# Kernel optimization log

Measured on AMD Instinct MI355X. Metric: run time of the kernel, lower is better.

## Reference

```python
import jax, jax.numpy as jnp
import numpy as np

D_MODEL = 768; HEADS = 12; DEPTH = 12; PATCH = 16; IMG = 224; NCLS = 1000
N_PATCH = (IMG // PATCH) ** 2  # 196
N_TOK = N_PATCH + 1            # 197 (cls token)
REGION = 16                    # tokens per routing region
TOPK = 4                       # regions gathered per query region


def layernorm(x, g, b, eps=1e-5):
    mu = jnp.mean(x, -1, keepdims=True)
    var = jnp.mean((x - mu) ** 2, -1, keepdims=True)
    return (x - mu) * jax.lax.rsqrt(var + eps) * g + b


def biformer_attn(h, qkv_w, qkv_b, proj_w, proj_b):
    # Bi-Level Routing Attention: region-mean routing + top-k region gather.
    B, N, C = h.shape
    dh = C // HEADS
    qkv = h @ qkv_w + qkv_b                      # [B,N,3C]
    pad = (-N) % REGION
    qkv = jnp.pad(qkv, ((0, 0), (0, pad), (0, 0)))
    Np = N + pad; R = Np // REGION
    q, k, v = jnp.split(qkv, 3, axis=-1)
    qr = q.reshape(B, R, REGION, C)
    kr = k.reshape(B, R, REGION, C)
    vr = v.reshape(B, R, REGION, C)
    # coarse region-level affinity from region means
    q_reg = qr.mean(2); k_reg = kr.mean(2)       # [B,R,C]
    aff = jnp.einsum('brc,bsc->brs', q_reg, k_reg)
    _, idx = jax.lax.top_k(aff, TOPK)            # [B,R,TOPK] int32
    gather = jax.vmap(lambda t, i: t[i])         # gather regions per batch elem
    kg = gather(kr, idx).reshape(B, R, TOPK * REGION, C)
    vg = gather(vr, idx).reshape(B, R, TOPK * REGION, C)
    # fine-grained attention within each region over gathered keys
    qh = qr.reshape(B, R, REGION, HEADS, dh)
    kh = kg.reshape(B, R, TOPK * REGION, HEADS, dh)
    vh = vg.reshape(B, R, TOPK * REGION, HEADS, dh)
    att = jnp.einsum('brmhd,brnhd->bhrmn', qh, kh) * (dh ** -0.5)
    att = jax.nn.softmax(att, axis=-1)
    out = jnp.einsum('bhrmn,brnhd->brmhd', att, vh).reshape(B, Np, C)[:, :N]
    return out @ proj_w + proj_b


def _forward(x, conv_w, conv_b, cls_token, pos_embed,
             ln1_g, ln1_b, qkv_w, qkv_b, proj_w, proj_b,
             ln2_g, ln2_b, fc1_w, fc1_b, fc2_w, fc2_b, head_w, head_b):
    B = x.shape[0]
    p = jax.lax.conv_general_dilated(
        x, conv_w, (PATCH, PATCH), 'VALID',
        dimension_numbers=('NCHW', 'OIHW', 'NCHW')) + conv_b[None, :, None, None]
    t = p.reshape(B, D_MODEL, N_PATCH).transpose(0, 2, 1)   # [B,196,C]
    t = jnp.concatenate([jnp.broadcast_to(cls_token, (B, 1, D_MODEL)), t], axis=1)
    t = t + pos_embed                                        # [B,197,C]

    def block(xc, pp):
        g1, b1, qw, qb, pw, pb, g2, b2, f1w, f1b, f2w, f2b = pp
        h = layernorm(xc, g1, b1)
        h = biformer_attn(h, qw, qb, pw, pb)
        h = layernorm(h, g2, b2)
        h = jax.nn.gelu(h @ f1w + f1b, approximate=False) @ f2w + f2b
        return xc + h, None   # single residual around LN-Attn-LN-MLP (as in source)

    blk = (ln1_g, ln1_b, qkv_w, qkv_b, proj_w, proj_b,
           ln2_g, ln2_b, fc1_w, fc1_b, fc2_w, fc2_b)
    t, _ = jax.lax.scan(block, t, blk)
    return t[:, 0] @ head_w + head_b


def setup_inputs() -> dict:
    key = jax.random.key(0)
    ks = jax.random.split(key, 10)
    B = 16; s = 0.02
    f32 = jnp.float32
    return {
        'x': jax.random.normal(ks[0], (B, 3, IMG, IMG), f32),
        'conv_w': jax.random.normal(ks[1], (D_MODEL, 3, PATCH, PATCH), f32) * s,
        'conv_b': jnp.zeros((D_MODEL,), f32),
        'cls_token': jax.random.normal(ks[2], (1, 1, D_MODEL), f32) * s,
        'pos_embed': jax.random.normal(ks[3], (1, N_TOK, D_MODEL), f32) * s,
        'ln1_g': jnp.ones((DEPTH, D_MODEL), f32),
        'ln1_b': jnp.zeros((DEPTH, D_MODEL), f32),
        'qkv_w': jax.random.normal(ks[4], (DEPTH, D_MODEL, 3 * D_MODEL), f32) * s,
        'qkv_b': jnp.zeros((DEPTH, 3 * D_MODEL), f32),
        'proj_w': jax.random.normal(ks[5], (DEPTH, D_MODEL, D_MODEL), f32) * s,
        'proj_b': jnp.zeros((DEPTH, D_MODEL), f32),
        'ln2_g': jnp.ones((DEPTH, D_MODEL), f32),
        'ln2_b': jnp.zeros((DEPTH, D_MODEL), f32),
        'fc1_w': jax.random.normal(ks[6], (DEPTH, D_MODEL, 4 * D_MODEL), f32) * s,
        'fc1_b': jnp.zeros((DEPTH, 4 * D_MODEL), f32),
        'fc2_w': jax.random.normal(ks[7], (DEPTH, 4 * D_MODEL, D_MODEL), f32) * s,
        'fc2_b': jnp.zeros((DEPTH, D_MODEL), f32),
        'head_w': jax.random.normal(ks[8], (D_MODEL, NCLS), f32) * s,
        'head_b': jnp.zeros((NCLS,), f32),
    }


def reference(x, conv_w, conv_b, cls_token, pos_embed,
              ln1_g, ln1_b, qkv_w, qkv_b, proj_w, proj_b,
              ln2_g, ln2_b, fc1_w, fc1_b, fc2_w, fc2_b, head_w, head_b):
    return _forward(x, conv_w, conv_b, cls_token, pos_embed,
                    ln1_g, ln1_b, qkv_w, qkv_b, proj_w, proj_b,
                    ln2_g, ln2_b, fc1_w, fc1_b, fc2_w, fc2_b, head_w, head_b)
```

## Files before the change

### kernel.cpp

```cpp
#include <hip/hip_runtime.h>
#include <hip/hip_bf16.h>
#include <math.h>


typedef __bf16 bf16_t;
typedef __bf16 bf16x8 __attribute__((ext_vector_type(8)));
typedef __bf16 bf16x4 __attribute__((ext_vector_type(4)));
typedef __bf16 bf16x2v __attribute__((ext_vector_type(2)));
typedef float floatx4 __attribute__((ext_vector_type(4)));

static __device__ __forceinline__ float b2f(bf16_t x) { return (float)x; }
static __device__ __forceinline__ bf16_t f2b(float x) { return (bf16_t)x; }

#define AS1q __attribute__((address_space(1)))
#define AS3q __attribute__((address_space(3)))
static __device__ __forceinline__ void gll16(const bf16_t* g, bf16_t* l) {
    __builtin_amdgcn_global_load_lds((const AS1q void*)g, (AS3q void*)l, 16, 0, 0);
}

__global__ void transpose_split(const float* __restrict__ in, bf16_t* __restrict__ oh,
                                bf16_t* __restrict__ ol, int R, int C) {
    __shared__ float tile[32][33];
    int c0 = blockIdx.x * 32, r0 = blockIdx.y * 32;
    int tx = threadIdx.x, ty = threadIdx.y;
#pragma unroll
    for (int i = 0; i < 4; i++) {
        int r = r0 + ty + i * 8;
        float v = 0.f;
        if (r < R && (c0 + tx) < C) v = in[(size_t)r * C + c0 + tx];
        tile[ty + i * 8][tx] = v;
    }
    __syncthreads();
#pragma unroll
    for (int i = 0; i < 4; i++) {
        int c = c0 + ty + i * 8;
        if (c < C && (r0 + tx) < R) {
            float v = tile[tx][ty + i * 8];
            bf16_t h = f2b(v);
            oh[(size_t)c * R + r0 + tx] = h;
            ol[(size_t)c * R + r0 + tx] = f2b(v - b2f(h));
        }
    }
}

__global__ void split_kernel(const float* __restrict__ in, bf16_t* __restrict__ oh,
                             bf16_t* __restrict__ ol, int n) {
    int id = blockIdx.x * 256 + threadIdx.x;
    if (id < n) {
        float v = in[id];
        bf16_t h = f2b(v);
        oh[id] = h;
        ol[id] = f2b(v - b2f(h));
    }
}

__global__ void im2col_split(const float* __restrict__ x, bf16_t* __restrict__ oh,
                             bf16_t* __restrict__ ol) {
    int id = blockIdx.x * 256 + threadIdx.x;
    if (id >= 3136 * 768) return;
    int col = id % 768, row = id / 768;
    int b = row / 196, p = row % 196;
    int py = p / 14, px = p % 14;
    int c = col >> 8, rem = col & 255, ky = rem >> 4, kx = rem & 15;
    float v = x[(((size_t)(b * 3 + c)) * 224 + (py * 16 + ky)) * 224 + (px * 16 + kx)];
    bf16_t h = f2b(v);
    oh[id] = h;
    ol[id] = f2b(v - b2f(h));
}

__global__ void clspos_kernel(const float* __restrict__ cls, const float* __restrict__ pos,
                              float* __restrict__ t) {
    int id = blockIdx.x * 256 + threadIdx.x;
    int b = id / 768, c = id % 768;
    t[((size_t)(b * 197)) * 768 + c] = cls[c] + pos[c];
}

__global__ __launch_bounds__(256) void ln_kernel(const float* __restrict__ in,
                                                 const float* __restrict__ g,
                                                 const float* __restrict__ bb,
                                                 bf16_t* __restrict__ oh,
                                                 bf16_t* __restrict__ ol,
                                                 float* __restrict__ outf) {
    int row = blockIdx.x;
    int t = threadIdx.x;
    const float* x = in + (size_t)row * 768;
    float v0 = x[t], v1 = x[t + 256], v2 = x[t + 512];
    float s = v0 + v1 + v2;
#pragma unroll
    for (int off = 32; off > 0; off >>= 1) s += __shfl_down(s, off, 64);
    __shared__ float red[8];
    int lane = t & 63, wave = t >> 6;
    if (lane == 0) red[wave] = s;
    __syncthreads();
    float mu = (red[0] + red[1] + red[2] + red[3]) * (1.f / 768.f);
    float d0 = v0 - mu, d1 = v1 - mu, d2 = v2 - mu;
    float vs = d0 * d0 + d1 * d1 + d2 * d2;
#pragma unroll
    for (int off = 32; off > 0; off >>= 1) vs += __shfl_down(vs, off, 64);
    if (lane == 0) red[4 + wave] = vs;
    __syncthreads();
    float var = (red[4] + red[5] + red[6] + red[7]) * (1.f / 768.f);
    float rstd = 1.0f / sqrtf(var + 1e-5f);
    float y0 = d0 * rstd * g[t] + bb[t];
    float y1 = d1 * rstd * g[t + 256] + bb[t + 256];
    float y2 = d2 * rstd * g[t + 512] + bb[t + 512];
    size_t base = (size_t)row * 768;
    bf16_t h0 = f2b(y0), h1 = f2b(y1), h2 = f2b(y2);
    oh[base + t] = h0; oh[base + t + 256] = h1; oh[base + t + 512] = h2;
    ol[base + t] = f2b(y0 - b2f(h0));
    ol[base + t + 256] = f2b(y1 - b2f(h1));
    ol[base + t + 512] = f2b(y2 - b2f(h2));
    if (outf) {
        outf[base + t] = y0; outf[base + t + 256] = y1; outf[base + t + 512] = y2;
    }
}

__global__ __launch_bounds__(256) void gemm_nts(const bf16_t* __restrict__ Ah,
                                                const bf16_t* __restrict__ Al,
                                                const bf16_t* __restrict__ Bh,
                                                const bf16_t* __restrict__ Bl,
                                                const float* __restrict__ bias,
                                                float* __restrict__ outF,
                                                bf16_t* __restrict__ outHi,
                                                bf16_t* __restrict__ outLo,
                                                int M, int N, int K, int Kc, int mode) {
    __shared__ __align__(16) bf16_t Ash[128 * 32];
    __shared__ __align__(16) bf16_t Asl[128 * 32];
    __shared__ __align__(16) bf16_t Bsh[128 * 32];
    __shared__ __align__(16) bf16_t Bsl[128 * 32];
    const int t = threadIdx.x;
    const int lane = t & 63, wave = t >> 6;
    const int quad = lane >> 4, l16 = lane & 15;
    const int wm = (wave >> 1) * 64, wn = (wave & 1) * 64;
    const int m0 = blockIdx.y * 128, n0 = blockIdx.x * 128;
    const int kz = blockIdx.z;

    floatx4 acc[4][4];
#pragma unroll
    for (int i = 0; i < 4; i++)
#pragma unroll
        for (int j = 0; j < 4; j++)
#pragma unroll
            for (int p = 0; p < 4; p++) acc[i][j][p] = 0.f;

    const int sr = wave * 16 + (lane >> 2);
    const int sc = (lane & 3) * 8;
    const size_t a0 = (size_t)(m0 + sr) * K + sc;
    const size_t a1 = (size_t)(m0 + 64 + sr) * K + sc;
    const size_t b0 = (size_t)(n0 + sr) * K + sc;
    const size_t b1 = (size_t)(n0 + 64 + sr) * K + sc;
    const int lo0 = wave * 512;
    const int lo1 = 2048 + wave * 512;

    const int kend = kz * Kc + Kc;
    for (int k0 = kz * Kc; k0 < kend; k0 += 32) {
        __syncthreads();
        gll16(Ah + a0 + k0, Ash + lo0);
        gll16(Ah + a1 + k0, Ash + lo1);
        gll16(Al + a0 + k0, Asl + lo0);
        gll16(Al + a1 + k0, Asl + lo1);
        gll16(Bh + b0 + k0, Bsh + lo0);
        gll16(Bh + b1 + k0, Bsh + lo1);
        gll16(Bl + b0 + k0, Bsl + lo0);
        gll16(Bl + b1 + k0, Bsl + lo1);
        __syncthreads();
        bf16x8 ah[4], al[4], bh[4], bl[4];
#pragma unroll
        for (int i = 0; i < 4; i++) {
            ah[i] = *(const bf16x8*)&Ash[(wm + i * 16 + l16) * 32 + quad * 8];
            al[i] = *(const bf16x8*)&Asl[(wm + i * 16 + l16) * 32 + quad * 8];
        }
#pragma unroll
        for (int j = 0; j < 4; j++) {
            bh[j] = *(const bf16x8*)&Bsh[(wn + j * 16 + l16) * 32 + quad * 8];
            bl[j] = *(const bf16x8*)&Bsl[(wn + j * 16 + l16) * 32 + quad * 8];
        }
#pragma unroll
        for (int i = 0; i < 4; i++)
#pragma unroll
            for (int j = 0; j < 4; j++) {
                acc[i][j] = __builtin_amdgcn_mfma_f32_16x16x32_bf16(ah[i], bh[j], acc[i][j], 0, 0, 0);
                acc[i][j] = __builtin_amdgcn_mfma_f32_16x16x32_bf16(ah[i], bl[j], acc[i][j], 0, 0, 0);
                acc[i][j] = __builtin_amdgcn_mfma_f32_16x16x32_bf16(al[i], bh[j], acc[i][j], 0, 0, 0);
            }
    }

    float* Pp = outF + (size_t)kz * ((size_t)M * (size_t)N);
#pragma unroll
    for (int i = 0; i < 4; i++) {
#pragma unroll
        for (int p = 0; p < 4; p++) {
            int m = m0 + wm + i * 16 + quad * 4 + p;
            if (m >= M) continue;
#pragma unroll
            for (int j = 0; j < 4; j++) {
                int n = n0 + wn + j * 16 + l16;
                if (n >= N) continue;
                if (mode == 0) {
                    Pp[(size_t)m * N + n] = acc[i][j][p];
                } else if (mode == 1) {
                    outF[(size_t)m * N + n] = acc[i][j][p] + bias[n];
                } else {
                    float v = acc[i][j][p] + bias[n];
                    float gl = 0.5f * v * (1.0f + erff(v * 0.70710678118654752f));
                    bf16_t h = f2b(gl);
                    outHi[(size_t)m * N + n] = h;
                    outLo[(size_t)m * N + n] = f2b(gl - b2f(h));
                }
            }
        }
    }
}

__global__ void reduce_kernel(const float* __restrict__ parts, int nchunks,
                              const float* __restrict__ bias, float* __restrict__ out,
                              const float* __restrict__ pos, int M, int N, int mode) {
    int id = blockIdx.x * 256 + threadIdx.x;
    int total = (M * N) >> 2;
    if (id >= total) return;
    size_t e = (size_t)id * 4;
    int n = (int)(e % N), m = (int)(e / N);
    size_t csz = (size_t)M * N;
    floatx4 s = *(const floatx4*)(parts + e);
    for (int c = 1; c < nchunks; c++) s += *(const floatx4*)(parts + (size_t)c * csz + e);
    s += *(const floatx4*)(bias + n);
    if (mode == 0) {
        *(floatx4*)(out + e) = s;
    } else if (mode == 1) {
        floatx4 o = *(const floatx4*)(out + e);
        *(floatx4*)(out + e) = o + s;
    } else {
        int b = m / 196, p = m % 196;
        floatx4 pv = *(const floatx4*)(pos + (size_t)(1 + p) * N + n);
        *(floatx4*)(out + ((size_t)(b * 197 + 1 + p)) * N + n) = s + pv;
    }
}

__global__ void regsum_kernel(const float* __restrict__ h, float* __restrict__ hsum) {
    int bid = blockIdx.x;
    int b = bid / 13, r = bid % 13;
    int t = threadIdx.x;
#pragma unroll
    for (int j = 0; j < 3; j++) {
        int c = t + j * 256;
        float s = 0.f;
        for (int tt = 0; tt < 16; tt++) {
            int tp = r * 16 + tt;
            if (tp < 197) s += h[((size_t)(b * 197 + tp)) * 768 + c];
        }
        hsum[(size_t)bid * 768 + c] = s;
    }
}

__global__ __launch_bounds__(256) void qkreg_gemm(const float* __restrict__ hsum,
                                                  const float* __restrict__ W,
                                                  const float* __restrict__ bias,
                                                  float* __restrict__ qreg,
                                                  float* __restrict__ kreg) {
    __shared__ float A_s[16][33];
    __shared__ float B_s[32][68];
    const int t = threadIdx.x;
    const int m0 = blockIdx.y * 16;
    const int n0 = blockIdx.x * 64;
    const int m = t >> 4;
    const int nn = (t & 15) * 4;
    floatx4 acc;
    acc[0] = acc[1] = acc[2] = acc[3] = 0.f;

    for (int k0 = 0; k0 < 768; k0 += 32) {
        {
            int c = (t & 15) * 2;
            A_s[t >> 4][c]     = hsum[(size_t)(m0 + (t >> 4)) * 768 + k0 + c];
            A_s[t >> 4][c + 1] = hsum[(size_t)(m0 + (t >> 4)) * 768 + k0 + c + 1];
        }
        {
            int kr = t >> 3, cc = (t & 7) * 8;
            const float* src = W + (size_t)(k0 + kr) * 2304 + n0 + cc;
            floatx4 w0 = *(const floatx4*)src;
            floatx4 w1 = *(const floatx4*)(src + 4);
            *(floatx4*)&B_s[kr][cc] = w0;
            *(floatx4*)&B_s[kr][cc + 4] = w1;
        }
        __syncthreads();
#pragma unroll
        for (int kk = 0; kk < 32; kk++) {
            float a = A_s[m][kk];
            floatx4 bv = *(const floatx4*)&B_s[kk][nn];
            acc += a * bv;
        }
        __syncthreads();
    }

    int row = m0 + m;
    int r = row % 13;
    float nr = (r == 12) ? 5.f : 16.f;
#pragma unroll
    for (int j = 0; j < 4; j++) {
        int c = n0 + nn + j;
        float val = (acc[j] + nr * bias[c]) * 0.0625f;
        if (c < 768) qreg[(size_t)row * 768 + c] = val;
        else         kreg[(size_t)row * 768 + (c - 768)] = val;
    }
}

__global__ __launch_bounds__(256) void aff_kernel(const float* __restrict__ qreg,
                                                  const float* __restrict__ kreg,
                                                  float* __restrict__ aff) {
    int wid = blockIdx.x * 4 + (threadIdx.x >> 6);
    int lane = threadIdx.x & 63;
    int s = wid % 13;
    int rem = wid / 13;
    int r = rem % 13, b = rem / 13;
    const float* qp = qreg + ((size_t)(b * 13 + r)) * 768;
    const float* kp = kreg + ((size_t)(b * 13 + s)) * 768;
    float a = 0.f;
#pragma unroll
    for (int jj = 0; jj < 3; jj++) {
        floatx4 q4 = *(const floatx4*)&qp[lane * 4 + jj * 256];
        floatx4 k4 = *(const floatx4*)&kp[lane * 4 + jj * 256];
        a += q4[0] * k4[0] + q4[1] * k4[1] + q4[2] * k4[2] + q4[3] * k4[3];
    }
#pragma unroll
    for (int msk = 32; msk >= 1; msk >>= 1) a += __shfl_xor(a, msk, 64);
    if (lane == 0) aff[wid] = a;
}

__global__ void topk_kernel(const float* __restrict__ aff, int* __restrict__ idx) {
    int tid = blockIdx.x * 256 + threadIdx.x;
    if (tid >= 208) return;
    const float* row = aff + (size_t)tid * 13;
    int mask = 0;
#pragma unroll
    for (int k = 0; k < 4; k++) {
        float best = -3.4e38f;
        int bi = 0;
        for (int s = 0; s < 13; s++) {
            if (!((mask >> s) & 1) && row[s] > best) { best = row[s]; bi = s; }
        }
        mask |= 1 << bi;
        idx[tid * 4 + k] = bi;
    }
}

__global__ __launch_bounds__(256) void attn_kernel(const float* __restrict__ qkv,
                                                   const int* __restrict__ idx,
                                                   bf16_t* __restrict__ oh,
                                                   bf16_t* __restrict__ ol) {
    __shared__ __align__(16) bf16_t Qh[16 * 72], Ql[16 * 72];
    __shared__ __align__(16) bf16_t Kh[64 * 72], Kl[64 * 72];
    __shared__ __align__(16) bf16_t Vth[64 * 68], Vtl[64 * 68];
    __shared__ __align__(16) float P_s[16 * 68];

    int bid = blockIdx.x;
    int head = bid % 12;
    int r = (bid / 12) % 13;
    int b = bid / (12 * 13);
    int t = threadIdx.x;
    const int lane = t & 63, wave = t >> 6;
    const int quad = lane >> 4, l16 = lane & 15;
    const int co = head * 64;
    const size_t rowb = (size_t)(b * 197);

    int regs[4];
#pragma unroll
    for (int j = 0; j < 4; j++) regs[j] = idx[(b * 13 + r) * 4 + j];

    {
        int rh = t >> 5;
        int c2 = (t & 31) * 2;
#pragma unroll
        for (int it = 0; it < 2; it++) {
            int m = rh + it * 8;
            int tp = r * 16 + m;
            float2 v; v.x = 0.f; v.y = 0.f;
            if (tp < 197) v = *(const float2*)&qkv[(rowb + tp) * 2304 + co + c2];
            bf16_t h0 = f2b(v.x), h1 = f2b(v.y);
            bf16x2v hh = {h0, h1};
            bf16x2v ll = {f2b(v.x - b2f(h0)), f2b(v.y - b2f(h1))};
            *(bf16x2v*)&Qh[m * 72 + c2] = hh;
            *(bf16x2v*)&Ql[m * 72 + c2] = ll;
        }
#pragma unroll
        for (int nb = 0; nb < 4; nb++) {
            int reg = regs[nb];
#pragma unroll
            for (int i2 = 0; i2 < 2; i2++) {
                int nn = rh + i2 * 8;
                int tp = reg * 16 + nn;
                int n = nb * 16 + nn;
                float2 v; v.x = 0.f; v.y = 0.f;
                if (tp < 197) v = *(const float2*)&qkv[(rowb + tp) * 2304 + 768 + co + c2];
                bf16_t h0 = f2b(v.x), h1 = f2b(v.y);
                bf16x2v hh = {h0, h1};
                bf16x2v ll = {f2b(v.x - b2f(h0)), f2b(v.y - b2f(h1))};
                *(bf16x2v*)&Kh[n * 72 + c2] = hh;
                *(bf16x2v*)&Kl[n * 72 + c2] = ll;
            }
        }
    }
    {
        int d = lane;
#pragma unroll
        for (int nb = 0; nb < 4; nb++) {
            int reg = regs[nb];
#pragma unroll
            for (int i2 = 0; i2 < 4; i2++) {
                int nn = wave + i2 * 4;
                int tp = reg * 16 + nn;
                int n = nb * 16 + nn;
                float v = (tp < 197) ? qkv[(rowb + tp) * 2304 + 1536 + co + d] : 0.f;
                bf16_t h = f2b(v);
                Vth[d * 68 + n] = h;
                Vtl[d * 68 + n] = f2b(v - b2f(h));
            }
        }
    }
    __syncthreads();

    {
        const int j = wave;
        bf16x8 qfh[2], qfl[2], kfh[2], kfl[2];
#pragma unroll
        for (int ks = 0; ks < 2; ks++) {
            qfh[ks] = *(const bf16x8*)&Qh[l16 * 72 + ks * 32 + quad * 8];
            qfl[ks] = *(const bf16x8*)&Ql[l16 * 72 + ks * 32 + quad * 8];
            kfh[ks] = *(const bf16x8*)&Kh[(j * 16 + l16) * 72 + ks * 32 + quad * 8];
            kfl[ks] = *(const bf16x8*)&Kl[(j * 16 + l16) * 72 + ks * 32 + quad * 8];
        }
        floatx4 s;
        s[0] = s[1] = s[2] = s[3] = 0.f;
#pragma unroll
        for (int ks = 0; ks < 2; ks++) {
            s = __builtin_amdgcn_mfma_f32_16x16x32_bf16(qfh[ks], kfh[ks], s, 0, 0, 0);
            s = __builtin_amdgcn_mfma_f32_16x16x32_bf16(qfh[ks], kfl[ks], s, 0, 0, 0);
            s = __builtin_amdgcn_mfma_f32_16x16x32_bf16(qfl[ks], kfh[ks], s, 0, 0, 0);
        }
#pragma unroll
        for (int p = 0; p < 4; p++)
            P_s[(quad * 4 + p) * 68 + j * 16 + l16] = s[p] * 0.125f;
    }
    __syncthreads();

    {
        int rw = t >> 4, c = t & 15;
        floatx4 v = *(const floatx4*)&P_s[rw * 68 + c * 4];
        float mx = fmaxf(fmaxf(v[0], v[1]), fmaxf(v[2], v[3]));
#pragma unroll
        for (int msk = 8; msk >= 1; msk >>= 1) mx = fmaxf(mx, __shfl_xor(mx, msk, 64));
        floatx4 e;
        e[0] = expf(v[0] - mx); e[1] = expf(v[1] - mx);
        e[2] = expf(v[2] - mx); e[3] = expf(v[3] - mx);
        float sm = e[0] + e[1] + e[2] + e[3];
#pragma unroll
        for (int msk = 8; msk >= 1; msk >>= 1) sm += __shfl_xor(sm, msk, 64);
        float inv = 1.f / sm;
        e[0] *= inv; e[1] *= inv; e[2] *= inv; e[3] *= inv;
        *(floatx4*)&P_s[rw * 68 + c * 4] = e;
    }
    __syncthreads();

    {
        const int j = wave;
        bf16x8 pfh[2], pfl[2], vfh[2], vfl[2];
#pragma unroll
        for (int ks = 0; ks < 2; ks++) {
            floatx4 p0 = *(const floatx4*)&P_s[l16 * 68 + ks * 32 + quad * 8];
            floatx4 p1 = *(const floatx4*)&P_s[l16 * 68 + ks * 32 + quad * 8 + 4];
#pragma unroll
            for (int i = 0; i < 4; i++) {
                float f0 = p0[i], f1 = p1[i];
                bf16_t h0 = f2b(f0), h1 = f2b(f1);
                pfh[ks][i] = h0;      pfh[ks][4 + i] = h1;
                pfl[ks][i] = f2b(f0 - b2f(h0));
                pfl[ks][4 + i] = f2b(f1 - b2f(h1));
            }
            int vrow = (j * 16 + l16) * 68 + ks * 32 + quad * 8;
            bf16x4 a0 = *(const bf16x4*)&Vth[vrow];
            bf16x4 a1 = *(const bf16x4*)&Vth[vrow + 4];
            bf16x4 c0 = *(const bf16x4*)&Vtl[vrow];
            bf16x4 c1 = *(const bf16x4*)&Vtl[vrow + 4];
#pragma unroll
            for (int i = 0; i < 4; i++) {
                vfh[ks][i] = a0[i]; vfh[ks][4 + i] = a1[i];
                vfl[ks][i] = c0[i]; vfl[ks][4 + i] = c1[i];
            }
        }
        floatx4 o;
        o[0] = o[1] = o[2] = o[3] = 0.f;
#pragma unroll
        for (int ks = 0; ks < 2; ks++) {
            o = __builtin_amdgcn_mfma_f32_16x16x32_bf16(pfh[ks], vfh[ks], o, 0, 0, 0);
            o = __builtin_amdgcn_mfma_f32_16x16x32_bf16(pfh[ks], vfl[ks], o, 0, 0, 0);
            o = __builtin_amdgcn_mfma_f32_16x16x32_bf16(pfl[ks], vfh[ks], o, 0, 0, 0);
        }
#pragma unroll
        for (int p = 0; p < 4; p++) {
            int m = quad * 4 + p;
            int tp = r * 16 + m;
            if (tp < 197) {
                size_t oidx = (rowb + tp) * 768 + co + j * 16 + l16;
                float f = o[p];
                bf16_t h = f2b(f);
                oh[oidx] = h;
                ol[oidx] = f2b(f - b2f(h));
            }
        }
    }
}

__global__ void headx_split(const float* __restrict__ t, bf16_t* __restrict__ oh,
                            bf16_t* __restrict__ ol) {
    int id = blockIdx.x * 256 + threadIdx.x;
    if (id >= 16 * 768) return;
    int b = id / 768, c = id % 768;
    float v = t[((size_t)(b * 197)) * 768 + c];
    bf16_t h = f2b(v);
    oh[id] = h;
    ol[id] = f2b(v - b2f(h));
}

extern "C" void kernel_launch(void* const* d_in, const int* in_sizes, int n_in,
                              void* d_out, int out_size, void* d_ws, size_t ws_size,
                              hipStream_t stream) {
    const float* x      = (const float*)d_in[0];
    const float* conv_w = (const float*)d_in[1];
    const float* conv_b = (const float*)d_in[2];
    const float* cls    = (const float*)d_in[3];
    const float* pos    = (const float*)d_in[4];
    const float* ln1g   = (const float*)d_in[5];
    const float* ln1b   = (const float*)d_in[6];
    const float* qkvw   = (const float*)d_in[7];
    const float* qkvb   = (const float*)d_in[8];
    const float* projw  = (const float*)d_in[9];
    const float* projb  = (const float*)d_in[10];
    const float* ln2g   = (const float*)d_in[11];
    const float* ln2b   = (const float*)d_in[12];
    const float* fc1w   = (const float*)d_in[13];
    const float* fc1b   = (const float*)d_in[14];
    const float* fc2w   = (const float*)d_in[15];
    const float* fc2b   = (const float*)d_in[16];
    const float* headw  = (const float*)d_in[17];
    const float* headb  = (const float*)d_in[18];
    float* out = (float*)d_out;

    char* ws = (char*)d_ws;
    size_t off = 0;
    auto alloc = [&](size_t bytes) -> void* {
        void* p = ws + off;
        off += (bytes + 255) & ~(size_t)255;
        return p;
    };
    float*  tbuf   = (float*)alloc((size_t)3152 * 768 * 4);
    float*  h32    = (float*)alloc((size_t)3152 * 768 * 4);
    bf16_t* lnHi   = (bf16_t*)alloc((size_t)3152 * 768 * 2);
    bf16_t* lnLo   = (bf16_t*)alloc((size_t)3152 * 768 * 2);
    bf16_t* atHi   = (bf16_t*)alloc((size_t)3152 * 768 * 2);
    bf16_t* atLo   = (bf16_t*)alloc((size_t)3152 * 768 * 2);
    bf16_t* WhiT   = (bf16_t*)alloc((size_t)3072 * 768 * 2);
    bf16_t* WloT   = (bf16_t*)alloc((size_t)3072 * 768 * 2);
    char*   uni    = (char*)alloc((size_t)3152 * 3072 * 2 * 2);
    float*  qkvF   = (float*)uni;
    bf16_t* geHi   = (bf16_t*)uni;
    bf16_t* geLo   = geHi + (size_t)3152 * 3072;
    bf16_t* imHi   = (bf16_t*)uni;
    bf16_t* imLo   = imHi + (size_t)3136 * 768;
    float*  embPar = (float*)(uni + (size_t)3136 * 768 * 2 * 2);
    float*  hsum   = (float*)alloc((size_t)208 * 768 * 4);
    float*  qreg   = (float*)alloc((size_t)208 * 768 * 4);
    float*  kreg   = (float*)alloc((size_t)208 * 768 * 4);
    float*  aff    = (float*)alloc((size_t)2704 * 4);
    int*    idx    = (int*)alloc((size_t)832 * 4);
    bf16_t* hdHi   = (bf16_t*)alloc((size_t)16 * 768 * 2);
    bf16_t* hdLo   = (bf16_t*)alloc((size_t)16 * 768 * 2);
    alloc((size_t)1 << 18);
    if (off > ws_size) return;

    dim3 blk(256);
    dim3 tblk(32, 8);
    const int RED768 = (3152 * 768 / 4) / 256;
    const int REDEMB = (3136 * 768 / 4) / 256;

    im2col_split<<<dim3(9408), blk, 0, stream>>>(x, imHi, imLo);
    split_kernel<<<dim3(2304), blk, 0, stream>>>(conv_w, WhiT, WloT, 768 * 768);
    gemm_nts<<<dim3(6, 25, 3), blk, 0, stream>>>(imHi, imLo, WhiT, WloT, nullptr,
                                                 embPar, nullptr, nullptr,
                                                 3136, 768, 768, 256, 0);
    reduce_kernel<<<dim3(REDEMB), blk, 0, stream>>>(embPar, 3, conv_b, tbuf, pos,
                                                    3136, 768, 2);
    clspos_kernel<<<dim3(48), blk, 0, stream>>>(cls, pos, tbuf);

    for (int l = 0; l < 12; l++) {
        ln_kernel<<<dim3(3152), blk, 0, stream>>>(tbuf, ln1g + l * 768, ln1b + l * 768,
                                                  lnHi, lnLo, h32);

        regsum_kernel<<<dim3(208), blk, 0, stream>>>(h32, hsum);
        qkreg_gemm<<<dim3(24, 13), blk, 0, stream>>>(hsum, qkvw + (size_t)l * 768 * 2304,
                                                     qkvb + l * 2304, qreg, kreg);
        aff_kernel<<<dim3(676), blk, 0, stream>>>(qreg, kreg, aff);
        topk_kernel<<<dim3(1), blk, 0, stream>>>(aff, idx);

        transpose_split<<<dim3(72, 24), tblk, 0, stream>>>(qkvw + (size_t)l * 768 * 2304,
                                                           WhiT, WloT, 768, 2304);
        gemm_nts<<<dim3(18, 25, 1), blk, 0, stream>>>(lnHi, lnLo, WhiT, WloT,
                                                      qkvb + l * 2304, qkvF,
                                                      nullptr, nullptr,
                                                      3152, 2304, 768, 768, 1);

        attn_kernel<<<dim3(16 * 13 * 12), blk, 0, stream>>>(qkvF, idx, atHi, atLo);

        transpose_split<<<dim3(24, 24), tblk, 0, stream>>>(projw + (size_t)l * 768 * 768,
                                                           WhiT, WloT, 768, 768);
        gemm_nts<<<dim3(6, 25, 4), blk, 0, stream>>>(atHi, atLo, WhiT, WloT, nullptr,
                                                     (float*)uni, nullptr, nullptr,
                                                     3152, 768, 768, 192, 0);
        reduce_kernel<<<dim3(RED768), blk, 0, stream>>>((float*)uni, 4, projb + l * 768,
                                                        h32, nullptr, 3152, 768, 0);

        ln_kernel<<<dim3(3152), blk, 0, stream>>>(h32, ln2g + l * 768, ln2b + l * 768,
                                                  lnHi, lnLo, (float*)nullptr);

        transpose_split<<<dim3(96, 24), tblk, 0, stream>>>(fc1w + (size_t)l * 768 * 3072,
                                                           WhiT, WloT, 768, 3072);
        gemm_nts<<<dim3(24, 25, 1), blk, 0, stream>>>(lnHi, lnLo, WhiT, WloT,
                                                      fc1b + l * 3072, nullptr,
                                                      geHi, geLo, 3152, 3072, 768, 768, 2);

        transpose_split<<<dim3(24, 96), tblk, 0, stream>>>(fc2w + (size_t)l * 3072 * 768,
                                                           WhiT, WloT, 3072, 768);
        gemm_nts<<<dim3(6, 25, 3), blk, 0, stream>>>(geHi, geLo, WhiT, WloT, nullptr,
                                                     h32, nullptr, nullptr,
                                                     3152, 768, 3072, 1024, 0);
        reduce_kernel<<<dim3(RED768), blk, 0, stream>>>(h32, 3, fc2b + l * 768,
                                                        tbuf, nullptr, 3152, 768, 1);
    }

    headx_split<<<dim3(48), blk, 0, stream>>>(tbuf, hdHi, hdLo);
    transpose_split<<<dim3(32, 24), tblk, 0, stream>>>(headw, WhiT, WloT, 768, 1000);
    gemm_nts<<<dim3(8, 1, 3), blk, 0, stream>>>(hdHi, hdLo, WhiT, WloT, nullptr,
                                                hsum, nullptr, nullptr,
                                                16, 1000, 768, 256, 0);
    reduce_kernel<<<dim3(16), blk, 0, stream>>>(hsum, 3, headb, out, nullptr,
                                                16, 1000, 0);
}
```

Measured before the change: 4.731 ms.

## Double-buffer GEMM LDS tiles and fuse reduce+LayerNorm and affinity+top-k kernels

The split-bf16 GEMM now keeps two LDS buffers. It issues global-to-LDS loads for the next K tile while MFMAs run on the current one, with one barrier per iteration instead of two. The split-K reduction after the projection GEMM is fused with the second LayerNorm, so the intermediate fp32 round trip and one launch go away. The region affinity and top-k kernels are merged into one 208-block kernel, which replaces the single-block top-k launch. Doubling LDS to 64KB per block may lower occupancy in the GEMM.

```diff
diff --git a/kernel.cpp b/kernel.cpp
--- a/kernel.cpp
+++ b/kernel.cpp
@@ -123,11 +123,12 @@
                                                 float* __restrict__ outF,
                                                 bf16_t* __restrict__ outHi,
                                                 bf16_t* __restrict__ outLo,
-                                                int M, int N, int K, int Kc, int mode) {
-    __shared__ __align__(16) bf16_t Ash[128 * 32];
-    __shared__ __align__(16) bf16_t Asl[128 * 32];
-    __shared__ __align__(16) bf16_t Bsh[128 * 32];
-    __shared__ __align__(16) bf16_t Bsl[128 * 32];
+                                                int M, int N, int K, int Kc,
+                                                size_t pstride, int mode) {
+    __shared__ __align__(16) bf16_t Ash[2][128 * 32];
+    __shared__ __align__(16) bf16_t Asl[2][128 * 32];
+    __shared__ __align__(16) bf16_t Bsh[2][128 * 32];
+    __shared__ __align__(16) bf16_t Bsl[2][128 * 32];
     const int t = threadIdx.x;
     const int lane = t & 63, wave = t >> 6;
     const int quad = lane >> 4, l16 = lane & 15;
@@ -152,28 +153,27 @@
     const int lo0 = wave * 512;
     const int lo1 = 2048 + wave * 512;
 
-    const int kend = kz * Kc + Kc;
-    for (int k0 = kz * Kc; k0 < kend; k0 += 32) {
-        __syncthreads();
-        gll16(Ah + a0 + k0, Ash + lo0);
-        gll16(Ah + a1 + k0, Ash + lo1);
-        gll16(Al + a0 + k0, Asl + lo0);
-        gll16(Al + a1 + k0, Asl + lo1);
-        gll16(Bh + b0 + k0, Bsh + lo0);
-        gll16(Bh + b1 + k0, Bsh + lo1);
-        gll16(Bl + b0 + k0, Bsl + lo0);
-        gll16(Bl + b1 + k0, Bsl + lo1);
-        __syncthreads();
+    auto stage = [&](int buf, int k) {
+        gll16(Ah + a0 + k, &Ash[buf][lo0]);
+        gll16(Ah + a1 + k, &Ash[buf][lo1]);
+        gll16(Al + a0 + k, &Asl[buf][lo0]);
+        gll16(Al + a1 + k, &Asl[buf][lo1]);
+        gll16(Bh + b0 + k, &Bsh[buf][lo0]);
+        gll16(Bh + b1 + k, &Bsh[buf][lo1]);
+        gll16(Bl + b0 + k, &Bsl[buf][lo0]);
+        gll16(Bl + b1 + k, &Bsl[buf][lo1]);
+    };
+    auto compute = [&](int buf) {
         bf16x8 ah[4], al[4], bh[4], bl[4];
 #pragma unroll
         for (int i = 0; i < 4; i++) {
-            ah[i] = *(const bf16x8*)&Ash[(wm + i * 16 + l16) * 32 + quad * 8];
-            al[i] = *(const bf16x8*)&Asl[(wm + i * 16 + l16) * 32 + quad * 8];
+            ah[i] = *(const bf16x8*)&Ash[buf][(wm + i * 16 + l16) * 32 + quad * 8];
+            al[i] = *(const bf16x8*)&Asl[buf][(wm + i * 16 + l16) * 32 + quad * 8];
         }
 #pragma unroll
         for (int j = 0; j < 4; j++) {
-            bh[j] = *(const bf16x8*)&Bsh[(wn + j * 16 + l16) * 32 + quad * 8];
-            bl[j] = *(const bf16x8*)&Bsl[(wn + j * 16 + l16) * 32 + quad * 8];
+            bh[j] = *(const bf16x8*)&Bsh[buf][(wn + j * 16 + l16) * 32 + quad * 8];
+            bl[j] = *(const bf16x8*)&Bsl[buf][(wn + j * 16 + l16) * 32 + quad * 8];
         }
 #pragma unroll
         for (int i = 0; i < 4; i++)
@@ -183,9 +183,21 @@
                 acc[i][j] = __builtin_amdgcn_mfma_f32_16x16x32_bf16(ah[i], bl[j], acc[i][j], 0, 0, 0);
                 acc[i][j] = __builtin_amdgcn_mfma_f32_16x16x32_bf16(al[i], bh[j], acc[i][j], 0, 0, 0);
             }
-    }
-
-    float* Pp = outF + (size_t)kz * ((size_t)M * (size_t)N);
+    };
+
+    const int kbeg = kz * Kc, kend = kbeg + Kc;
+    stage(0, kbeg);
+    __syncthreads();
+    int cur = 0;
+    for (int k0 = kbeg + 32; k0 < kend; k0 += 32) {
+        stage(cur ^ 1, k0);
+        compute(cur);
+        __syncthreads();
+        cur ^= 1;
+    }
+    compute(cur);
+
+    float* Pp = outF + (size_t)kz * pstride;
 #pragma unroll
     for (int i = 0; i < 4; i++) {
 #pragma unroll
@@ -236,6 +248,52 @@
     }
 }
 
+__global__ __launch_bounds__(256) void reduce_ln_kernel(const float* __restrict__ parts,
+                                                        int nchunks, size_t cstride,
+                                                        const float* __restrict__ bias,
+                                                        const float* __restrict__ g,
+                                                        const float* __restrict__ bb,
+                                                        bf16_t* __restrict__ oh,
+                                                        bf16_t* __restrict__ ol) {
+    int row = blockIdx.x;
+    int t = threadIdx.x;
+    float y0, y1, y2;
+    {
+        size_t base = (size_t)row * 768;
+        float a0 = bias[t], a1 = bias[t + 256], a2 = bias[t + 512];
+        for (int c = 0; c < nchunks; c++) {
+            const float* p = parts + (size_t)c * cstride + base;
+            a0 += p[t]; a1 += p[t + 256]; a2 += p[t + 512];
+        }
+        y0 = a0; y1 = a1; y2 = a2;
+    }
+    float s = y0 + y1 + y2;
+#pragma unroll
+    for (int off = 32; off > 0; off >>= 1) s += __shfl_down(s, off, 64);
+    __shared__ float red[8];
+    int lane = t & 63, wave = t >> 6;
+    if (lane == 0) red[wave] = s;
+    __syncthreads();
+    float mu = (red[0] + red[1] + red[2] + red[3]) * (1.f / 768.f);
+    float d0 = y0 - mu, d1 = y1 - mu, d2 = y2 - mu;
+    float vs = d0 * d0 + d1 * d1 + d2 * d2;
+#pragma unroll
+    for (int off = 32; off > 0; off >>= 1) vs += __shfl_down(vs, off, 64);
+    if (lane == 0) red[4 + wave] = vs;
+    __syncthreads();
+    float var = (red[4] + red[5] + red[6] + red[7]) * (1.f / 768.f);
+    float rstd = 1.0f / sqrtf(var + 1e-5f);
+    float z0 = d0 * rstd * g[t] + bb[t];
+    float z1 = d1 * rstd * g[t + 256] + bb[t + 256];
+    float z2 = d2 * rstd * g[t + 512] + bb[t + 512];
+    size_t base = (size_t)row * 768;
+    bf16_t h0 = f2b(z0), h1 = f2b(z1), h2 = f2b(z2);
+    oh[base + t] = h0; oh[base + t + 256] = h1; oh[base + t + 512] = h2;
+    ol[base + t] = f2b(z0 - b2f(h0));
+    ol[base + t + 256] = f2b(z1 - b2f(h1));
+    ol[base + t + 512] = f2b(z2 - b2f(h2));
+}
+
 __global__ void regsum_kernel(const float* __restrict__ h, float* __restrict__ hsum) {
     int bid = blockIdx.x;
     int b = bid / 13, r = bid % 13;
@@ -303,42 +361,40 @@
     }
 }
 
-__global__ __launch_bounds__(256) void aff_kernel(const float* __restrict__ qreg,
-                                                  const float* __restrict__ kreg,
-                                                  float* __restrict__ aff) {
-    int wid = blockIdx.x * 4 + (threadIdx.x >> 6);
-    int lane = threadIdx.x & 63;
-    int s = wid % 13;
-    int rem = wid / 13;
-    int r = rem % 13, b = rem / 13;
-    const float* qp = qreg + ((size_t)(b * 13 + r)) * 768;
-    const float* kp = kreg + ((size_t)(b * 13 + s)) * 768;
-    float a = 0.f;
-#pragma unroll
-    for (int jj = 0; jj < 3; jj++) {
-        floatx4 q4 = *(const floatx4*)&qp[lane * 4 + jj * 256];
-        floatx4 k4 = *(const floatx4*)&kp[lane * 4 + jj * 256];
-        a += q4[0] * k4[0] + q4[1] * k4[1] + q4[2] * k4[2] + q4[3] * k4[3];
-    }
-#pragma unroll
-    for (int msk = 32; msk >= 1; msk >>= 1) a += __shfl_xor(a, msk, 64);
-    if (lane == 0) aff[wid] = a;
-}
-
-__global__ void topk_kernel(const float* __restrict__ aff, int* __restrict__ idx) {
-    int tid = blockIdx.x * 256 + threadIdx.x;
-    if (tid >= 208) return;
-    const float* row = aff + (size_t)tid * 13;
-    int mask = 0;
-#pragma unroll
-    for (int k = 0; k < 4; k++) {
-        float best = -3.4e38f;
-        int bi = 0;
-        for (int s = 0; s < 13; s++) {
-            if (!((mask >> s) & 1) && row[s] > best) { best = row[s]; bi = s; }
-        }
-        mask |= 1 << bi;
-        idx[tid * 4 + k] = bi;
+__global__ __launch_bounds__(256) void afftopk_kernel(const float* __restrict__ qreg,
+                                                      const float* __restrict__ kreg,
+                                                      int* __restrict__ idx) {
+    __shared__ float arow[16];
+    int br = blockIdx.x;
+    int b = br / 13;
+    int t = threadIdx.x, lane = t & 63, w = t >> 6;
+    const float* qp = qreg + (size_t)br * 768;
+    for (int s = w; s < 13; s += 4) {
+        const float* kp = kreg + ((size_t)(b * 13 + s)) * 768;
+        float a = 0.f;
+#pragma unroll
+        for (int jj = 0; jj < 3; jj++) {
+            floatx4 q4 = *(const floatx4*)&qp[lane * 4 + jj * 256];
+            floatx4 k4 = *(const floatx4*)&kp[lane * 4 + jj * 256];
+            a += q4[0] * k4[0] + q4[1] * k4[1] + q4[2] * k4[2] + q4[3] * k4[3];
+        }
+#pragma unroll
+        for (int msk = 32; msk >= 1; msk >>= 1) a += __shfl_xor(a, msk, 64);
+        if (lane == 0) arow[s] = a;
+    }
+    __syncthreads();
+    if (t == 0) {
+        int mask = 0;
+#pragma unroll
+        for (int k = 0; k < 4; k++) {
+            float best = -3.4e38f;
+            int bi = 0;
+            for (int s = 0; s < 13; s++) {
+                if (!((mask >> s) & 1) && arow[s] > best) { best = arow[s]; bi = s; }
+            }
+            mask |= 1 << bi;
+            idx[br * 4 + k] = bi;
+        }
     }
 }
 
@@ -568,7 +624,6 @@
     float*  hsum   = (float*)alloc((size_t)208 * 768 * 4);
     float*  qreg   = (float*)alloc((size_t)208 * 768 * 4);
     float*  kreg   = (float*)alloc((size_t)208 * 768 * 4);
-    float*  aff    = (float*)alloc((size_t)2704 * 4);
     int*    idx    = (int*)alloc((size_t)832 * 4);
     bf16_t* hdHi   = (bf16_t*)alloc((size_t)16 * 768 * 2);
     bf16_t* hdLo   = (bf16_t*)alloc((size_t)16 * 768 * 2);
@@ -579,12 +634,13 @@
     dim3 tblk(32, 8);
     const int RED768 = (3152 * 768 / 4) / 256;
     const int REDEMB = (3136 * 768 / 4) / 256;
+    const size_t PS = (size_t)3152 * 768;
 
     im2col_split<<<dim3(9408), blk, 0, stream>>>(x, imHi, imLo);
     split_kernel<<<dim3(2304), blk, 0, stream>>>(conv_w, WhiT, WloT, 768 * 768);
     gemm_nts<<<dim3(6, 25, 3), blk, 0, stream>>>(imHi, imLo, WhiT, WloT, nullptr,
                                                  embPar, nullptr, nullptr,
-                                                 3136, 768, 768, 256, 0);
+                                                 3136, 768, 768, 256, (size_t)3136 * 768, 0);
     reduce_kernel<<<dim3(REDEMB), blk, 0, stream>>>(embPar, 3, conv_b, tbuf, pos,
                                                     3136, 768, 2);
     clspos_kernel<<<dim3(48), blk, 0, stream>>>(cls, pos, tbuf);
@@ -596,15 +652,14 @@
         regsum_kernel<<<dim3(208), blk, 0, stream>>>(h32, hsum);
         qkreg_gemm<<<dim3(24, 13), blk, 0, stream>>>(hsum, qkvw + (size_t)l * 768 * 2304,
                                                      qkvb + l * 2304, qreg, kreg);
-        aff_kernel<<<dim3(676), blk, 0, stream>>>(qreg, kreg, aff);
-        topk_kernel<<<dim3(1), blk, 0, stream>>>(aff, idx);
+        afftopk_kernel<<<dim3(208), blk, 0, stream>>>(qreg, kreg, idx);
 
         transpose_split<<<dim3(72, 24), tblk, 0, stream>>>(qkvw + (size_t)l * 768 * 2304,
                                                            WhiT, WloT, 768, 2304);
         gemm_nts<<<dim3(18, 25, 1), blk, 0, stream>>>(lnHi, lnLo, WhiT, WloT,
                                                       qkvb + l * 2304, qkvF,
                                                       nullptr, nullptr,
-                                                      3152, 2304, 768, 768, 1);
+                                                      3152, 2304, 768, 768, 0, 1);
 
         attn_kernel<<<dim3(16 * 13 * 12), blk, 0, stream>>>(qkvF, idx, atHi, atLo);
 
@@ -612,24 +667,23 @@
                                                            WhiT, WloT, 768, 768);
         gemm_nts<<<dim3(6, 25, 4), blk, 0, stream>>>(atHi, atLo, WhiT, WloT, nullptr,
                                                      (float*)uni, nullptr, nullptr,
-                                                     3152, 768, 768, 192, 0);
-        reduce_kernel<<<dim3(RED768), blk, 0, stream>>>((float*)uni, 4, projb + l * 768,
-                                                        h32, nullptr, 3152, 768, 0);
-
-        ln_kernel<<<dim3(3152), blk, 0, stream>>>(h32, ln2g + l * 768, ln2b + l * 768,
-                                                  lnHi, lnLo, (float*)nullptr);
+                                                     3152, 768, 768, 192, PS, 0);
+        reduce_ln_kernel<<<dim3(3152), blk, 0, stream>>>((float*)uni, 4, PS,
+                                                         projb + l * 768,
+                                                         ln2g + l * 768, ln2b + l * 768,
+                                                         lnHi, lnLo);
 
         transpose_split<<<dim3(96, 24), tblk, 0, stream>>>(fc1w + (size_t)l * 768 * 3072,
                                                            WhiT, WloT, 768, 3072);
         gemm_nts<<<dim3(24, 25, 1), blk, 0, stream>>>(lnHi, lnLo, WhiT, WloT,
                                                       fc1b + l * 3072, nullptr,
-                                                      geHi, geLo, 3152, 3072, 768, 768, 2);
+                                                      geHi, geLo, 3152, 3072, 768, 768, 0, 2);
 
         transpose_split<<<dim3(24, 96), tblk, 0, stream>>>(fc2w + (size_t)l * 3072 * 768,
                                                            WhiT, WloT, 3072, 768);
         gemm_nts<<<dim3(6, 25, 3), blk, 0, stream>>>(geHi, geLo, WhiT, WloT, nullptr,
                                                      h32, nullptr, nullptr,
-                                                     3152, 768, 3072, 1024, 0);
+                                                     3152, 768, 3072, 1024, PS, 0);
         reduce_kernel<<<dim3(RED768), blk, 0, stream>>>(h32, 3, fc2b + l * 768,
                                                         tbuf, nullptr, 3152, 768, 1);
     }
@@ -638,7 +692,7 @@
     transpose_split<<<dim3(32, 24), tblk, 0, stream>>>(headw, WhiT, WloT, 768, 1000);
     gemm_nts<<<dim3(8, 1, 3), blk, 0, stream>>>(hdHi, hdLo, WhiT, WloT, nullptr,
                                                 hsum, nullptr, nullptr,
-                                                16, 1000, 768, 256, 0);
+                                                16, 1000, 768, 256, (size_t)16 * 1000, 0);
     reduce_kernel<<<dim3(16), blk, 0, stream>>>(hsum, 3, headb, out, nullptr,
                                                 16, 1000, 0);
 }
```

After: 5.240 ms. 10.8% more time.
